# Optimization experiments

Measured on AMD Instinct MI355X. Metric: run time of the kernel, lower is better.

Reference implementation:

```python
import jax, jax.numpy as jnp
import numpy as np

H = 1024   # hidden_size
S = 32768  # seq_len


def setup_inputs() -> dict:
    key = jax.random.key(0)
    k1, k2, k3, k4 = jax.random.split(key, 4)
    scale = 1.0 / np.sqrt(H)
    return {
        "hidden": jax.random.normal(k1, (H,), dtype=jnp.float32),
        "encoder_outputs": jax.random.normal(k2, (S, H), dtype=jnp.float32),
        "W": jax.random.normal(k3, (H, H), dtype=jnp.float32) * scale,
        "b": jax.random.normal(k4, (H,), dtype=jnp.float32) * scale,
    }


def reference(hidden, encoder_outputs, W, b):
    # method == 'general': energy_i = W @ enc_i + b ; score_i = hidden . energy_i
    # Vectorized: scores = (enc @ W^T + b) @ hidden  -> [S]
    energies = jnp.einsum("sh,dh->sd", encoder_outputs, W) + b  # [S, H]
    scores = energies @ hidden                                   # [S]
    attn = jax.nn.softmax(scores)                                 # softmax over seq_len
    return attn[None, None, :]                                    # [1, 1, S]
```

## Files before the change

kernel.cpp:

```cpp
#include <hip/hip_runtime.h>
#include <math.h>

#define H 1024
#define S 32768

#define WS_V      0
#define WS_SCORES 1024
#define WS_STATS  (1024 + S)

__global__ __launch_bounds__(256) void matvec_wt_h(const float* __restrict__ W,
                                                   const float* __restrict__ hidden,
                                                   float* __restrict__ v) {
    const int h  = blockIdx.x * 256 + threadIdx.x;
    const int d0 = blockIdx.y * 64;
    float acc = 0.f;
#pragma unroll 8
    for (int i = 0; i < 64; ++i) {
        const int d = d0 + i;
        acc += W[(size_t)d * H + h] * hidden[d];
    }
    atomicAdd(&v[h], acc);
}

__global__ __launch_bounds__(256) void scores_kernel(const float* __restrict__ enc,
                                                     const float* __restrict__ v,
                                                     float* __restrict__ scores) {
    const int lane = threadIdx.x & 63;
    const int wave = threadIdx.x >> 6;
    const int wavesPerBlock = blockDim.x >> 6;
    const int globalWave = blockIdx.x * wavesPerBlock + wave;
    const int numWaves   = gridDim.x * wavesPerBlock;

    const float4* v4 = (const float4*)v;
    float4 vf[4];
#pragma unroll
    for (int k = 0; k < 4; ++k) vf[k] = v4[lane + 64 * k];

    for (int row = globalWave; row < S; row += numWaves) {
        const float4* e4 = (const float4*)(enc + (size_t)row * H);
        float acc = 0.f;
#pragma unroll
        for (int k = 0; k < 4; ++k) {
            const float4 e = e4[lane + 64 * k];
            acc += e.x * vf[k].x + e.y * vf[k].y + e.z * vf[k].z + e.w * vf[k].w;
        }
#pragma unroll
        for (int off = 32; off > 0; off >>= 1)
            acc += __shfl_xor(acc, off, 64);
        if (lane == 0) scores[row] = acc;
    }
}

__global__ __launch_bounds__(1024) void softmax_stats(const float* __restrict__ scores,
                                                      float* __restrict__ stats) {
    __shared__ float redm[16];
    __shared__ float reds[16];
    const int tid  = threadIdx.x;
    const int lane = tid & 63;
    const int wv   = tid >> 6;

    float local[32];
    float m = -INFINITY;
#pragma unroll
    for (int i = 0; i < 32; ++i) {
        local[i] = scores[tid + i * 1024];
        m = fmaxf(m, local[i]);
    }
#pragma unroll
    for (int off = 32; off > 0; off >>= 1)
        m = fmaxf(m, __shfl_xor(m, off, 64));
    if (lane == 0) redm[wv] = m;
    __syncthreads();
    float bm = redm[0];
#pragma unroll
    for (int i = 1; i < 16; ++i) bm = fmaxf(bm, redm[i]);

    float s = 0.f;
#pragma unroll
    for (int i = 0; i < 32; ++i) s += __expf(local[i] - bm);
#pragma unroll
    for (int off = 32; off > 0; off >>= 1)
        s += __shfl_xor(s, off, 64);
    if (lane == 0) reds[wv] = s;
    __syncthreads();
    if (tid == 0) {
        float ts = 0.f;
#pragma unroll
        for (int i = 0; i < 16; ++i) ts += reds[i];
        stats[0] = bm;
        stats[1] = ts;
    }
}

__global__ __launch_bounds__(256) void normalize_kernel(const float* __restrict__ scores,
                                                        const float* __restrict__ stats,
                                                        float* __restrict__ out) {
    const int i = blockIdx.x * 256 + threadIdx.x;
    const float m  = stats[0];
    const float rs = 1.0f / stats[1];
    out[i] = __expf(scores[i] - m) * rs;
}

extern "C" void kernel_launch(void* const* d_in, const int* in_sizes, int n_in,
                              void* d_out, int out_size, void* d_ws, size_t ws_size,
                              hipStream_t stream) {
    const float* hidden = (const float*)d_in[0];
    const float* enc    = (const float*)d_in[1];
    const float* W      = (const float*)d_in[2];
    float* out = (float*)d_out;

    float* ws     = (float*)d_ws;
    float* v      = ws + WS_V;
    float* scores = ws + WS_SCORES;
    float* stats  = ws + WS_STATS;

    hipMemsetAsync(v, 0, H * sizeof(float), stream);

    dim3 g1(H / 256, 16);
    matvec_wt_h<<<g1, 256, 0, stream>>>(W, hidden, v);

    scores_kernel<<<1024, 256, 0, stream>>>(enc, v, scores);

    softmax_stats<<<1, 1024, 0, stream>>>(scores, stats);

    normalize_kernel<<<S / 256, 256, 0, stream>>>(scores, stats, out);
}
```

Measured before the change: 208.6 us.

## Fuse online softmax stats into scores kernel and drop memset and atomics

The matvec now writes per-slice partial sums instead of using atomics, so the memset is no longer needed. The scores kernel reduces those partials into shared memory and computes per-block online-softmax max and sum. The single-block stats kernel is removed: each finalize block re-reduces the 1024 per-block stats redundantly and then normalizes. This cuts launches from five operations to three and removes the serial single-block reduction, at the cost of each scores block re-reading 64KB of partials.

```diff
diff --git a/kernel.cpp b/kernel.cpp
--- a/kernel.cpp
+++ b/kernel.cpp
@@ -3,102 +3,136 @@
 
 #define H 1024
 #define S 32768
+#define NPART 16
 
-#define WS_V      0
-#define WS_SCORES 1024
-#define WS_STATS  (1024 + S)
+#define WS_PART   0
+#define WS_SCORES 16384
+#define WS_PM     (16384 + S)
+#define WS_PS     (16384 + S + 1024)
 
-__global__ __launch_bounds__(256) void matvec_wt_h(const float* __restrict__ W,
-                                                   const float* __restrict__ hidden,
-                                                   float* __restrict__ v) {
+__global__ __launch_bounds__(256) void matvec_partial(const float* __restrict__ W,
+                                                      const float* __restrict__ hidden,
+                                                      float* __restrict__ ws) {
+    float* part = ws + WS_PART;
     const int h  = blockIdx.x * 256 + threadIdx.x;
-    const int d0 = blockIdx.y * 64;
+    const int by = blockIdx.y;
+    const int d0 = by * 64;
     float acc = 0.f;
 #pragma unroll 8
     for (int i = 0; i < 64; ++i) {
         const int d = d0 + i;
         acc += W[(size_t)d * H + h] * hidden[d];
     }
-    atomicAdd(&v[h], acc);
+    part[by * H + h] = acc;
 }
 
-__global__ __launch_bounds__(256) void scores_kernel(const float* __restrict__ enc,
-                                                     const float* __restrict__ v,
-                                                     float* __restrict__ scores) {
-    const int lane = threadIdx.x & 63;
-    const int wave = threadIdx.x >> 6;
-    const int wavesPerBlock = blockDim.x >> 6;
-    const int globalWave = blockIdx.x * wavesPerBlock + wave;
-    const int numWaves   = gridDim.x * wavesPerBlock;
+__global__ __launch_bounds__(256) void scores_partial(const float* __restrict__ enc,
+                                                      float* __restrict__ ws) {
+    float* part   = ws + WS_PART;
+    float* scores = ws + WS_SCORES;
+    float* pm     = ws + WS_PM;
+    float* ps     = ws + WS_PS;
 
-    const float4* v4 = (const float4*)v;
+    const int tid  = threadIdx.x;
+    const int lane = tid & 63;
+    const int wv   = tid >> 6;
+    const int blk  = blockIdx.x;
+
+    __shared__ float vsh[H];
+    {
+        const float4* p4 = (const float4*)part;
+        float4 a = make_float4(0.f, 0.f, 0.f, 0.f);
+#pragma unroll
+        for (int p = 0; p < NPART; ++p) {
+            const float4 w = p4[p * (H / 4) + tid];
+            a.x += w.x; a.y += w.y; a.z += w.z; a.w += w.w;
+        }
+        ((float4*)vsh)[tid] = a;
+    }
+    __syncthreads();
+
+    const float4* v4 = (const float4*)vsh;
     float4 vf[4];
 #pragma unroll
     for (int k = 0; k < 4; ++k) vf[k] = v4[lane + 64 * k];
 
-    for (int row = globalWave; row < S; row += numWaves) {
+    const int gw = blk * 4 + wv;
+    float mw = -INFINITY, sw = 0.f;
+#pragma unroll
+    for (int it = 0; it < 8; ++it) {
+        const int row = gw * 8 + it;
         const float4* e4 = (const float4*)(enc + (size_t)row * H);
-        float acc = 0.f;
+        float a = 0.f;
 #pragma unroll
         for (int k = 0; k < 4; ++k) {
             const float4 e = e4[lane + 64 * k];
-            acc += e.x * vf[k].x + e.y * vf[k].y + e.z * vf[k].z + e.w * vf[k].w;
+            a += e.x * vf[k].x + e.y * vf[k].y + e.z * vf[k].z + e.w * vf[k].w;
         }
 #pragma unroll
         for (int off = 32; off > 0; off >>= 1)
-            acc += __shfl_xor(acc, off, 64);
-        if (lane == 0) scores[row] = acc;
+            a += __shfl_xor(a, off, 64);
+        if (lane == 0) scores[row] = a;
+        const float nm = fmaxf(mw, a);
+        sw = sw * __expf(mw - nm) + __expf(a - nm);
+        mw = nm;
+    }
+
+    __shared__ float sm[4], ss[4];
+    if (lane == 0) { sm[wv] = mw; ss[wv] = sw; }
+    __syncthreads();
+    if (tid == 0) {
+        float m = sm[0], s = ss[0];
+#pragma unroll
+        for (int i = 1; i < 4; ++i) {
+            const float nm = fmaxf(m, sm[i]);
+            s = s * __expf(m - nm) + ss[i] * __expf(sm[i] - nm);
+            m = nm;
+        }
+        pm[blk] = m; ps[blk] = s;
     }
 }
 
-__global__ __launch_bounds__(1024) void softmax_stats(const float* __restrict__ scores,
-                                                      float* __restrict__ stats) {
-    __shared__ float redm[16];
-    __shared__ float reds[16];
+__global__ __launch_bounds__(256) void finalize(const float* __restrict__ ws,
+                                                float* __restrict__ out) {
+    const float* scores = ws + WS_SCORES;
+    const float* pm     = ws + WS_PM;
+    const float* ps     = ws + WS_PS;
+
     const int tid  = threadIdx.x;
     const int lane = tid & 63;
     const int wv   = tid >> 6;
 
-    float local[32];
-    float m = -INFINITY;
+    float m = -INFINITY, s = 0.f;
 #pragma unroll
-    for (int i = 0; i < 32; ++i) {
-        local[i] = scores[tid + i * 1024];
-        m = fmaxf(m, local[i]);
+    for (int i = 0; i < 4; ++i) {
+        const int idx = tid + i * 256;
+        const float om = pm[idx], os = ps[idx];
+        const float nm = fmaxf(m, om);
+        s = s * __expf(m - nm) + os * __expf(om - nm);
+        m = nm;
     }
 #pragma unroll
-    for (int off = 32; off > 0; off >>= 1)
-        m = fmaxf(m, __shfl_xor(m, off, 64));
-    if (lane == 0) redm[wv] = m;
+    for (int off = 32; off > 0; off >>= 1) {
+        const float om = __shfl_xor(m, off, 64);
+        const float os = __shfl_xor(s, off, 64);
+        const float nm = fmaxf(m, om);
+        s = s * __expf(m - nm) + os * __expf(om - nm);
+        m = nm;
+    }
+    __shared__ float sm[4], ss[4];
+    if (lane == 0) { sm[wv] = m; ss[wv] = s; }
     __syncthreads();
-    float bm = redm[0];
+    float M = sm[0], Ssum = ss[0];
 #pragma unroll
-    for (int i = 1; i < 16; ++i) bm = fmaxf(bm, redm[i]);
+    for (int i = 1; i < 4; ++i) {
+        const float nm = fmaxf(M, sm[i]);
+        Ssum = Ssum * __expf(M - nm) + ss[i] * __expf(sm[i] - nm);
+        M = nm;
+    }
+    const float rs = 1.0f / Ssum;
 
-    float s = 0.f;
-#pragma unroll
-    for (int i = 0; i < 32; ++i) s += __expf(local[i] - bm);
-#pragma unroll
-    for (int off = 32; off > 0; off >>= 1)
-        s += __shfl_xor(s, off, 64);
-    if (lane == 0) reds[wv] = s;
-    __syncthreads();
-    if (tid == 0) {
-        float ts = 0.f;
-#pragma unroll
-        for (int i = 0; i < 16; ++i) ts += reds[i];
-        stats[0] = bm;
-        stats[1] = ts;
-    }
-}
-
-__global__ __launch_bounds__(256) void normalize_kernel(const float* __restrict__ scores,
-                                                        const float* __restrict__ stats,
-                                                        float* __restrict__ out) {
-    const int i = blockIdx.x * 256 + threadIdx.x;
-    const float m  = stats[0];
-    const float rs = 1.0f / stats[1];
-    out[i] = __expf(scores[i] - m) * rs;
+    const int i = blockIdx.x * 256 + tid;
+    out[i] = __expf(scores[i] - M) * rs;
 }
 
 extern "C" void kernel_launch(void* const* d_in, const int* in_sizes, int n_in,
@@ -108,20 +142,9 @@
     const float* enc    = (const float*)d_in[1];
     const float* W      = (const float*)d_in[2];
     float* out = (float*)d_out;
+    float* ws  = (float*)d_ws;
 
-    float* ws     = (float*)d_ws;
-    float* v      = ws + WS_V;
-    float* scores = ws + WS_SCORES;
-    float* stats  = ws + WS_STATS;
-
-    hipMemsetAsync(v, 0, H * sizeof(float), stream);
-
-    dim3 g1(H / 256, 16);
-    matvec_wt_h<<<g1, 256, 0, stream>>>(W, hidden, v);
-
-    scores_kernel<<<1024, 256, 0, stream>>>(enc, v, scores);
-
-    softmax_stats<<<1, 1024, 0, stream>>>(scores, stats);
-
-    normalize_kernel<<<S / 256, 256, 0, stream>>>(scores, stats, out);
+    matvec_partial<<<dim3(H / 256, NPART), 256, 0, stream>>>(W, hidden, ws);
+    scores_partial<<<1024, 256, 0, stream>>>(enc, ws);
+    finalize<<<S / 256, 256, 0, stream>>>(ws, out);
 }
```

After: 207.7 us. No clear change (-0.4%).
